# Performance work log

Hardware: AMD Instinct MI355X
Metric: run time of the kernel (lower is better)

The kernel has to match this reference:

```python
import jax, jax.numpy as jnp
import numpy as np

N_SEGMENT = 8
NUM_HEADS = 4
KERNEL = 5
PAD_L = 4  # causal left padding (kernel_size - 1)


def setup_inputs() -> dict:
    key = jax.random.key(0)
    k1, k2 = jax.random.split(key)
    x = jax.random.normal(k1, (128, 512, 14, 14), dtype=jnp.float32)
    W_weight = jax.random.normal(k2, (NUM_HEADS * KERNEL, 512), dtype=jnp.float32) * 0.02
    return {"x": x, "W_weight": W_weight}


def reference(x, W_weight):
    nt, c, h, w = x.shape
    T = N_SEGMENT
    n = nt // T
    B = n * h * w
    H, K, R = NUM_HEADS, KERNEL, c // NUM_HEADS

    # (nt, c, h, w) -> (n, T, c, h, w) -> permute(1,0,3,4,2) -> (T, B, c)
    xt = x.reshape(n, T, c, h, w).transpose(1, 0, 3, 4, 2).reshape(T, B, c)

    # per-position dynamic kernels: Linear(c -> H*K), softmax over kernel taps
    w_logits = jnp.einsum('tbc,oc->tbo', xt, W_weight).reshape(T, B, H, K)
    weights = jax.nn.softmax(w_logits, axis=-1)  # (T, B, H, K)

    # causal banded unfold: window[t, ..., k] = x[t + k - PAD_L], zeros outside
    xpad = jnp.pad(xt, ((PAD_L, 0), (0, 0), (0, 0)))  # (T+4, B, c)
    windows = jnp.stack([xpad[k:k + T] for k in range(K)], axis=-1)  # (T, B, c, K)
    win = windows.reshape(T, B, H, R, K)

    out = jnp.einsum('tbhrk,tbhk->tbhr', win, weights).reshape(T, B, c)

    # (T, n, h, w, c) -> permute(1,0,4,2,3) -> (nt, c, h, w)
    out = out.reshape(T, n, h, w, c).transpose(1, 0, 4, 2, 3).reshape(nt, c, h, w)
    return out
```

## Files before the change

kernel.cpp:

```cpp
#include <hip/hip_runtime.h>

#define T 8
#define C 512
#define HW 196
#define NSEG 16
#define NT (NSEG * T)
#define B_TOT (NSEG * HW)
#define NH 4
#define KK 5
#define NO 20
#define S_SPLIT 8
#define CCH (C / S_SPLIT)

__global__ __launch_bounds__(256) void k_logits(const float* __restrict__ x,
                                                const float* __restrict__ W,
                                                float* __restrict__ pl) {
    const int idx = blockIdx.x * 256 + threadIdx.x;
    const int nt  = idx / HW;
    const int hw  = idx - nt * HW;
    const int s   = blockIdx.y;
    const int cbase = s * CCH;

    const float* xp = x + ((size_t)nt * C + cbase) * HW + hw;

    float acc[NO];
#pragma unroll
    for (int o = 0; o < NO; ++o) acc[o] = 0.f;

    float xv[8], xn[8];
#pragma unroll
    for (int u = 0; u < 8; ++u) xv[u] = xp[u * HW];

#pragma unroll
    for (int c0 = 0; c0 < CCH; c0 += 8) {
        if (c0 + 8 < CCH) {
#pragma unroll
            for (int u = 0; u < 8; ++u) xn[u] = xp[(c0 + 8 + u) * HW];
        }
        const float* wr = W + cbase + c0;
#pragma unroll
        for (int o = 0; o < NO; ++o) {
#pragma unroll
            for (int u = 0; u < 8; ++u)
                acc[o] = fmaf(xv[u], wr[o * C + u], acc[o]);
        }
#pragma unroll
        for (int u = 0; u < 8; ++u) xv[u] = xn[u];
    }

    float* pp = pl + ((size_t)(s * NT + nt) * NO) * HW + hw;
#pragma unroll
    for (int o = 0; o < NO; ++o) pp[o * HW] = acc[o];
}

__global__ __launch_bounds__(256) void k_softmax(const float* __restrict__ pl,
                                                 float* __restrict__ wgt) {
    const int b = blockIdx.x * 256 + threadIdx.x;
    const int t = blockIdx.y;
    const int h = blockIdx.z;
    if (b >= B_TOT) return;
    const int n  = b / HW;
    const int hw = b - n * HW;
    const int nt = n * T + t;

    float lg[KK];
#pragma unroll
    for (int k = 0; k < KK; ++k) {
        float sm = 0.f;
#pragma unroll
        for (int s = 0; s < S_SPLIT; ++s)
            sm += pl[((size_t)(s * NT + nt) * NO + h * KK + k) * HW + hw];
        lg[k] = sm;
    }

    float m = lg[0];
#pragma unroll
    for (int k = 1; k < KK; ++k) m = fmaxf(m, lg[k]);
    float e[KK];
    float sum = 0.f;
#pragma unroll
    for (int k = 0; k < KK; ++k) {
        e[k] = __expf(lg[k] - m);
        sum += e[k];
    }
    const float r = 1.f / sum;
#pragma unroll
    for (int k = 0; k < KK; ++k)
        wgt[((size_t)((t * NH + h) * KK + k)) * B_TOT + b] = e[k] * r;
}

__global__ __launch_bounds__(256) void k_conv(const float* __restrict__ x,
                                              const float* __restrict__ wgt,
                                              float* __restrict__ out) {
    const int idx = blockIdx.x * 256 + threadIdx.x;
    const int hw  = idx % HW;
    const int t1  = idx / HW;
    const int c   = t1 % C;
    const int n   = t1 / C;
    const int h   = c >> 7;
    const int b   = n * HW + hw;

    float w[T][KK];
#pragma unroll
    for (int t = 0; t < T; ++t)
#pragma unroll
        for (int k = 0; k < KK; ++k)
            w[t][k] = wgt[((size_t)((t * NH + h) * KK + k)) * B_TOT + b];

    const size_t base = ((size_t)(n * T) * C + c) * HW + hw;
    float xv[T];
#pragma unroll
    for (int t = 0; t < T; ++t) xv[t] = x[base + (size_t)t * C * HW];

#pragma unroll
    for (int t = 0; t < T; ++t) {
        float acc = 0.f;
#pragma unroll
        for (int k = 0; k < KK; ++k) {
            const int j = t + k - 4;
            if (j >= 0) acc = fmaf(w[t][k], xv[j], acc);
        }
        out[base + (size_t)t * C * HW] = acc;
    }
}

extern "C" void kernel_launch(void* const* d_in, const int* in_sizes, int n_in,
                              void* d_out, int out_size, void* d_ws, size_t ws_size,
                              hipStream_t stream) {
    const float* x = (const float*)d_in[0];
    const float* W = (const float*)d_in[1];
    float* out = (float*)d_out;

    float* pl  = (float*)d_ws;
    float* wgt = pl + (size_t)S_SPLIT * NT * NO * HW;

    k_logits<<<dim3(25088 / 256, S_SPLIT), 256, 0, stream>>>(x, W, pl);
    k_softmax<<<dim3((B_TOT + 255) / 256, T, NH), 256, 0, stream>>>(pl, wgt);
    k_conv<<<dim3((NSEG * C * HW) / 256), 256, 0, stream>>>(x, wgt, out);
}
```

Before: 125.8 us.

## Fuse logits split-K reduction and softmax via LDS; vectorize conv with float4

The separate logits and softmax kernels are merged into one kernel. Eight wavefronts each handle a 64-channel slice, and their partial logits are reduced in shared memory, so the partial-logit buffer no longer makes a round trip through global memory and one launch is removed. The conv kernel now handles four spatial positions per thread using float4 loads and stores, which cuts the number of memory instructions. The cost is heavier LDS use and more synchronisation per block. Vectorised access relies on HW=196 being divisible by 4 for alignment.

New measurement: 144.1 us. 14.5% more time.

```diff
diff --git a/kernel.cpp b/kernel.cpp
--- a/kernel.cpp
+++ b/kernel.cpp
@@ -9,118 +9,131 @@
 #define NH 4
 #define KK 5
 #define NO 20
-#define S_SPLIT 8
-#define CCH (C / S_SPLIT)
+#define LDS_STRIDE 21
 
-__global__ __launch_bounds__(256) void k_logits(const float* __restrict__ x,
-                                                const float* __restrict__ W,
-                                                float* __restrict__ pl) {
-    const int idx = blockIdx.x * 256 + threadIdx.x;
+__global__ __launch_bounds__(512) void k_fused(const float* __restrict__ x,
+                                               const float* __restrict__ W,
+                                               float* __restrict__ wgt) {
+    const int tid = threadIdx.x;
+    const int p   = tid & 63;
+    const int s   = __builtin_amdgcn_readfirstlane(tid >> 6);
+
+    const int idx = blockIdx.x * 64 + p;
     const int nt  = idx / HW;
     const int hw  = idx - nt * HW;
-    const int s   = blockIdx.y;
-    const int cbase = s * CCH;
 
-    const float* xp = x + ((size_t)nt * C + cbase) * HW + hw;
+    __shared__ float lds[8 * 64 * LDS_STRIDE];
+    __shared__ float lds2[NO * 64];
+
+    const float* xp = x + ((size_t)nt * C + s * 64) * HW + hw;
+    const float* Wp = W + s * 64;
 
     float acc[NO];
 #pragma unroll
     for (int o = 0; o < NO; ++o) acc[o] = 0.f;
 
-    float xv[8], xn[8];
+    float xv[2][8];
 #pragma unroll
-    for (int u = 0; u < 8; ++u) xv[u] = xp[u * HW];
+    for (int u = 0; u < 8; ++u) xv[0][u] = xp[u * HW];
 
 #pragma unroll
-    for (int c0 = 0; c0 < CCH; c0 += 8) {
-        if (c0 + 8 < CCH) {
-#pragma unroll
-            for (int u = 0; u < 8; ++u) xn[u] = xp[(c0 + 8 + u) * HW];
-        }
-        const float* wr = W + cbase + c0;
-#pragma unroll
-        for (int o = 0; o < NO; ++o) {
+    for (int cb = 0; cb < 8; ++cb) {
+        const int cur = cb & 1;
+        if (cb + 1 < 8) {
 #pragma unroll
             for (int u = 0; u < 8; ++u)
-                acc[o] = fmaf(xv[u], wr[o * C + u], acc[o]);
+                xv[cur ^ 1][u] = xp[((cb + 1) * 8 + u) * HW];
         }
+        __builtin_amdgcn_sched_barrier(0);
+        const float* wr = Wp + cb * 8;
 #pragma unroll
-        for (int u = 0; u < 8; ++u) xv[u] = xn[u];
+        for (int o = 0; o < NO; ++o)
+#pragma unroll
+            for (int u = 0; u < 8; ++u)
+                acc[o] = fmaf(xv[cur][u], wr[o * C + u], acc[o]);
     }
 
-    float* pp = pl + ((size_t)(s * NT + nt) * NO) * HW + hw;
+    float* lp = &lds[(s * 64 + p) * LDS_STRIDE];
 #pragma unroll
-    for (int o = 0; o < NO; ++o) pp[o * HW] = acc[o];
-}
+    for (int o = 0; o < NO; ++o) lp[o] = acc[o];
+    __syncthreads();
 
-__global__ __launch_bounds__(256) void k_softmax(const float* __restrict__ pl,
-                                                 float* __restrict__ wgt) {
-    const int b = blockIdx.x * 256 + threadIdx.x;
-    const int t = blockIdx.y;
-    const int h = blockIdx.z;
-    if (b >= B_TOT) return;
-    const int n  = b / HW;
-    const int hw = b - n * HW;
-    const int nt = n * T + t;
-
-    float lg[KK];
-#pragma unroll
-    for (int k = 0; k < KK; ++k) {
+    for (int i = tid; i < NO * 64; i += 512) {
+        const int o = i >> 6, pp = i & 63;
         float sm = 0.f;
 #pragma unroll
-        for (int s = 0; s < S_SPLIT; ++s)
-            sm += pl[((size_t)(s * NT + nt) * NO + h * KK + k) * HW + hw];
-        lg[k] = sm;
+        for (int s2 = 0; s2 < 8; ++s2)
+            sm += lds[(s2 * 64 + pp) * LDS_STRIDE + o];
+        lds2[o * 64 + pp] = sm;
     }
+    __syncthreads();
 
-    float m = lg[0];
+    if (tid < 256) {
+        const int pp = tid & 63;
+        const int h  = tid >> 6;
+        float lg[KK];
 #pragma unroll
-    for (int k = 1; k < KK; ++k) m = fmaxf(m, lg[k]);
-    float e[KK];
-    float sum = 0.f;
+        for (int k = 0; k < KK; ++k) lg[k] = lds2[(h * KK + k) * 64 + pp];
+        float m = lg[0];
 #pragma unroll
-    for (int k = 0; k < KK; ++k) {
-        e[k] = __expf(lg[k] - m);
-        sum += e[k];
+        for (int k = 1; k < KK; ++k) m = fmaxf(m, lg[k]);
+        float e[KK], sum = 0.f;
+#pragma unroll
+        for (int k = 0; k < KK; ++k) { e[k] = __expf(lg[k] - m); sum += e[k]; }
+        const float r = 1.f / sum;
+#pragma unroll
+        for (int k = 0; k < KK; ++k) lds2[(h * KK + k) * 64 + pp] = e[k] * r;
     }
-    const float r = 1.f / sum;
-#pragma unroll
-    for (int k = 0; k < KK; ++k)
-        wgt[((size_t)((t * NH + h) * KK + k)) * B_TOT + b] = e[k] * r;
+    __syncthreads();
+
+    for (int i = tid; i < NO * 64; i += 512) {
+        const int o  = i >> 6, pp = i & 63;
+        const int id = blockIdx.x * 64 + pp;
+        const int nt2 = id / HW;
+        const int hw2 = id - nt2 * HW;
+        const int n2 = nt2 >> 3, t2 = nt2 & 7;
+        const int b  = n2 * HW + hw2;
+        wgt[(size_t)(t2 * NO + o) * B_TOT + b] = lds2[o * 64 + pp];
+    }
 }
 
 __global__ __launch_bounds__(256) void k_conv(const float* __restrict__ x,
                                               const float* __restrict__ wgt,
                                               float* __restrict__ out) {
-    const int idx = blockIdx.x * 256 + threadIdx.x;
-    const int hw  = idx % HW;
-    const int t1  = idx / HW;
-    const int c   = t1 % C;
-    const int n   = t1 / C;
-    const int h   = c >> 7;
-    const int b   = n * HW + hw;
+    const int flat = blockIdx.x * 256 + threadIdx.x;
+    const int q    = flat % 49;
+    const int rest = flat / 49;
+    const int c    = rest & 511;
+    const int n    = rest >> 9;
+    const int h    = c >> 7;
+    const int hw   = q * 4;
+    const int b    = n * HW + hw;
 
-    float w[T][KK];
+    const size_t xbase = ((size_t)(n * T) * C + c) * HW + hw;
+
+    float4 xv[T];
 #pragma unroll
     for (int t = 0; t < T; ++t)
-#pragma unroll
-        for (int k = 0; k < KK; ++k)
-            w[t][k] = wgt[((size_t)((t * NH + h) * KK + k)) * B_TOT + b];
-
-    const size_t base = ((size_t)(n * T) * C + c) * HW + hw;
-    float xv[T];
-#pragma unroll
-    for (int t = 0; t < T; ++t) xv[t] = x[base + (size_t)t * C * HW];
+        xv[t] = *(const float4*)&x[xbase + (size_t)t * C * HW];
 
 #pragma unroll
     for (int t = 0; t < T; ++t) {
-        float acc = 0.f;
+        float4 w4[KK];
+#pragma unroll
+        for (int k = 0; k < KK; ++k)
+            w4[k] = *(const float4*)&wgt[(size_t)((t * NH + h) * KK + k) * B_TOT + b];
+        float4 a = make_float4(0.f, 0.f, 0.f, 0.f);
 #pragma unroll
         for (int k = 0; k < KK; ++k) {
             const int j = t + k - 4;
-            if (j >= 0) acc = fmaf(w[t][k], xv[j], acc);
+            if (j >= 0) {
+                a.x = fmaf(w4[k].x, xv[j].x, a.x);
+                a.y = fmaf(w4[k].y, xv[j].y, a.y);
+                a.z = fmaf(w4[k].z, xv[j].z, a.z);
+                a.w = fmaf(w4[k].w, xv[j].w, a.w);
+            }
         }
-        out[base + (size_t)t * C * HW] = acc;
+        *(float4*)&out[xbase + (size_t)t * C * HW] = a;
     }
 }
 
@@ -131,10 +144,8 @@
     const float* W = (const float*)d_in[1];
     float* out = (float*)d_out;
 
-    float* pl  = (float*)d_ws;
-    float* wgt = pl + (size_t)S_SPLIT * NT * NO * HW;
+    float* wgt = (float*)d_ws;
 
-    k_logits<<<dim3(25088 / 256, S_SPLIT), 256, 0, stream>>>(x, W, pl);
-    k_softmax<<<dim3((B_TOT + 255) / 256, T, NH), 256, 0, stream>>>(pl, wgt);
-    k_conv<<<dim3((NSEG * C * HW) / 256), 256, 0, stream>>>(x, wgt, out);
+    k_fused<<<dim3(25088 / 64), 512, 0, stream>>>(x, W, wgt);
+    k_conv<<<dim3((NSEG * C * 49) / 256), 256, 0, stream>>>(x, wgt, out);
 }
```

## Reduce logits in LDS across waves, reshape partial layout, and amortize conv weights

Applied to the files above, without the earlier changes.

The logits kernel now gives each of the four waves in a block a 32-channel slice for the same 64 positions. The four partial sums are reduced through LDS before one write per split, so the channel splits written to the workspace drop from 8 to 4. The partial-logit layout becomes output-major over positions, so the softmax reads contiguously and fewer blocks are launched. The conv kernel now handles four channels per thread, reusing the 40 loaded softmax weights instead of reloading them per channel. In exchange there is extra LDS traffic and a barrier in the logits kernel, and fewer threads in the conv kernel with more registers each.

New measurement: 142.7 us. 1.13x slower.

```diff
diff --git a/kernel.cpp b/kernel.cpp
--- a/kernel.cpp
+++ b/kernel.cpp
@@ -6,62 +6,76 @@
 #define NSEG 16
 #define NT (NSEG * T)
 #define B_TOT (NSEG * HW)
+#define NPOS (NT * HW)
 #define NH 4
 #define KK 5
 #define NO 20
-#define S_SPLIT 8
-#define CCH (C / S_SPLIT)
+#define S_SPLIT 4
+#define LDS_STRIDE 21
 
 __global__ __launch_bounds__(256) void k_logits(const float* __restrict__ x,
                                                 const float* __restrict__ W,
                                                 float* __restrict__ pl) {
-    const int idx = blockIdx.x * 256 + threadIdx.x;
+    const int tid = threadIdx.x;
+    const int p   = tid & 63;
+    const int wv  = __builtin_amdgcn_readfirstlane(tid >> 6);
+    const int s   = blockIdx.y;
+
+    const int idx = blockIdx.x * 64 + p;
     const int nt  = idx / HW;
     const int hw  = idx - nt * HW;
-    const int s   = blockIdx.y;
-    const int cbase = s * CCH;
+    const int cb  = s * 128 + wv * 32;
 
-    const float* xp = x + ((size_t)nt * C + cbase) * HW + hw;
+    __shared__ float lds[4 * 64 * LDS_STRIDE];
+
+    const float* xp = x + ((size_t)nt * C + cb) * HW + hw;
+    const float* Wp = W + cb;
 
     float acc[NO];
 #pragma unroll
     for (int o = 0; o < NO; ++o) acc[o] = 0.f;
 
-    float xv[8], xn[8];
+    float xv[2][8];
 #pragma unroll
-    for (int u = 0; u < 8; ++u) xv[u] = xp[u * HW];
+    for (int u = 0; u < 8; ++u) xv[0][u] = xp[u * HW];
 
 #pragma unroll
-    for (int c0 = 0; c0 < CCH; c0 += 8) {
-        if (c0 + 8 < CCH) {
-#pragma unroll
-            for (int u = 0; u < 8; ++u) xn[u] = xp[(c0 + 8 + u) * HW];
-        }
-        const float* wr = W + cbase + c0;
-#pragma unroll
-        for (int o = 0; o < NO; ++o) {
+    for (int bt = 0; bt < 4; ++bt) {
+        const int cur = bt & 1;
+        if (bt + 1 < 4) {
 #pragma unroll
             for (int u = 0; u < 8; ++u)
-                acc[o] = fmaf(xv[u], wr[o * C + u], acc[o]);
+                xv[cur ^ 1][u] = xp[((bt + 1) * 8 + u) * HW];
         }
+        __builtin_amdgcn_sched_barrier(0);
+        const float* wr = Wp + bt * 8;
 #pragma unroll
-        for (int u = 0; u < 8; ++u) xv[u] = xn[u];
+        for (int o = 0; o < NO; ++o)
+#pragma unroll
+            for (int u = 0; u < 8; ++u)
+                acc[o] = fmaf(xv[cur][u], wr[o * C + u], acc[o]);
     }
 
-    float* pp = pl + ((size_t)(s * NT + nt) * NO) * HW + hw;
+    float* lp = &lds[(wv * 64 + p) * LDS_STRIDE];
 #pragma unroll
-    for (int o = 0; o < NO; ++o) pp[o * HW] = acc[o];
+    for (int o = 0; o < NO; ++o) lp[o] = acc[o];
+    __syncthreads();
+
+    for (int i = tid; i < NO * 64; i += 256) {
+        const int o = i >> 6, pp = i & 63;
+        float sm = 0.f;
+#pragma unroll
+        for (int w2 = 0; w2 < 4; ++w2)
+            sm += lds[(w2 * 64 + pp) * LDS_STRIDE + o];
+        pl[((size_t)(s * NO + o)) * NPOS + blockIdx.x * 64 + pp] = sm;
+    }
 }
 
 __global__ __launch_bounds__(256) void k_softmax(const float* __restrict__ pl,
                                                  float* __restrict__ wgt) {
-    const int b = blockIdx.x * 256 + threadIdx.x;
-    const int t = blockIdx.y;
-    const int h = blockIdx.z;
-    if (b >= B_TOT) return;
-    const int n  = b / HW;
-    const int hw = b - n * HW;
-    const int nt = n * T + t;
+    const int f   = blockIdx.x * 256 + threadIdx.x;
+    const int h   = f / NPOS;
+    const int idx = f - h * NPOS;
 
     float lg[KK];
 #pragma unroll
@@ -69,21 +83,22 @@
         float sm = 0.f;
 #pragma unroll
         for (int s = 0; s < S_SPLIT; ++s)
-            sm += pl[((size_t)(s * NT + nt) * NO + h * KK + k) * HW + hw];
+            sm += pl[((size_t)(s * NO + h * KK + k)) * NPOS + idx];
         lg[k] = sm;
     }
 
     float m = lg[0];
 #pragma unroll
     for (int k = 1; k < KK; ++k) m = fmaxf(m, lg[k]);
-    float e[KK];
-    float sum = 0.f;
+    float e[KK], sum = 0.f;
 #pragma unroll
-    for (int k = 0; k < KK; ++k) {
-        e[k] = __expf(lg[k] - m);
-        sum += e[k];
-    }
+    for (int k = 0; k < KK; ++k) { e[k] = __expf(lg[k] - m); sum += e[k]; }
     const float r = 1.f / sum;
+
+    const int nt = idx / HW;
+    const int hw = idx - nt * HW;
+    const int n  = nt >> 3, t = nt & 7;
+    const int b  = n * HW + hw;
 #pragma unroll
     for (int k = 0; k < KK; ++k)
         wgt[((size_t)((t * NH + h) * KK + k)) * B_TOT + b] = e[k] * r;
@@ -92,13 +107,14 @@
 __global__ __launch_bounds__(256) void k_conv(const float* __restrict__ x,
                                               const float* __restrict__ wgt,
                                               float* __restrict__ out) {
-    const int idx = blockIdx.x * 256 + threadIdx.x;
-    const int hw  = idx % HW;
-    const int t1  = idx / HW;
-    const int c   = t1 % C;
-    const int n   = t1 / C;
-    const int h   = c >> 7;
-    const int b   = n * HW + hw;
+    const int f  = blockIdx.x * 256 + threadIdx.x;
+    const int hw = f % HW;
+    const int r  = f / HW;
+    const int cg = r & 127;
+    const int n  = r >> 7;
+    const int c0 = cg * 4;
+    const int h  = cg >> 5;
+    const int b  = n * HW + hw;
 
     float w[T][KK];
 #pragma unroll
@@ -107,20 +123,22 @@
         for (int k = 0; k < KK; ++k)
             w[t][k] = wgt[((size_t)((t * NH + h) * KK + k)) * B_TOT + b];
 
-    const size_t base = ((size_t)(n * T) * C + c) * HW + hw;
-    float xv[T];
 #pragma unroll
-    for (int t = 0; t < T; ++t) xv[t] = x[base + (size_t)t * C * HW];
-
+    for (int ci = 0; ci < 4; ++ci) {
+        const size_t base = ((size_t)(n * T) * C + (c0 + ci)) * HW + hw;
+        float xv[T];
 #pragma unroll
-    for (int t = 0; t < T; ++t) {
-        float acc = 0.f;
+        for (int t = 0; t < T; ++t) xv[t] = x[base + (size_t)t * C * HW];
 #pragma unroll
-        for (int k = 0; k < KK; ++k) {
-            const int j = t + k - 4;
-            if (j >= 0) acc = fmaf(w[t][k], xv[j], acc);
+        for (int t = 0; t < T; ++t) {
+            float a = 0.f;
+#pragma unroll
+            for (int k = 0; k < KK; ++k) {
+                const int j = t + k - 4;
+                if (j >= 0) a = fmaf(w[t][k], xv[j], a);
+            }
+            out[base + (size_t)t * C * HW] = a;
         }
-        out[base + (size_t)t * C * HW] = acc;
     }
 }
 
@@ -132,9 +150,9 @@
     float* out = (float*)d_out;
 
     float* pl  = (float*)d_ws;
-    float* wgt = pl + (size_t)S_SPLIT * NT * NO * HW;
+    float* wgt = pl + (size_t)S_SPLIT * NO * NPOS;
 
-    k_logits<<<dim3(25088 / 256, S_SPLIT), 256, 0, stream>>>(x, W, pl);
-    k_softmax<<<dim3((B_TOT + 255) / 256, T, NH), 256, 0, stream>>>(pl, wgt);
-    k_conv<<<dim3((NSEG * C * HW) / 256), 256, 0, stream>>>(x, wgt, out);
+    k_logits<<<dim3(NPOS / 64, S_SPLIT), 256, 0, stream>>>(x, W, pl);
+    k_softmax<<<dim3(NH * NPOS / 256), 256, 0, stream>>>(pl, wgt);
+    k_conv<<<dim3(NSEG * 128 * HW / 256), 256, 0, stream>>>(x, wgt, out);
 }
```
